# Kernel tuning notes

Measured on AMD Instinct MI355X. Metric: run time of the kernel, lower is better.

## Reference

```python
import jax, jax.numpy as jnp
import numpy as np

INPUT_SIZE, HIDDEN_SIZE, OUTPUT_SIZE = 256, 512, 256
BATCH, SEQ_LEN = 64, 1024


def _xavier(key, shape):
    fan_out, fan_in = shape
    limit = float(np.sqrt(6.0 / (fan_in + fan_out)))
    return jax.random.uniform(key, shape, jnp.float32, -limit, limit)


def setup_inputs() -> dict:
    key = jax.random.key(0)
    k_x, k_w1, k_w2 = jax.random.split(key, 3)
    x = jax.random.normal(k_x, (BATCH, SEQ_LEN, INPUT_SIZE), jnp.float32)
    W_ih = _xavier(k_w1, (HIDDEN_SIZE, INPUT_SIZE + HIDDEN_SIZE))  # torch Linear weight [out, in]
    b_ih = jnp.zeros((HIDDEN_SIZE,), jnp.float32)
    W_ho = _xavier(k_w2, (OUTPUT_SIZE, HIDDEN_SIZE))
    b_ho = jnp.zeros((OUTPUT_SIZE,), jnp.float32)
    return {"x": x, "W_ih": W_ih, "b_ih": b_ih, "W_ho": W_ho, "b_ho": b_ho}


def reference(x, W_ih, b_ih, W_ho, b_ho):
    batch, seq_len, input_size = x.shape
    hidden = W_ih.shape[0]
    # Split concat-linear into two matmuls: [x_t, h] @ W^T = x_t @ Wx^T + h @ Wh^T
    Wx = W_ih[:, :input_size]   # [H, I]
    Wh = W_ih[:, input_size:]   # [H, H]
    # Precompute input projections for all timesteps: [S, B, H]
    x_proj = jnp.einsum('bsi,hi->sbh', x, Wx) + b_ih

    def step(h, xp_t):
        h_new = jnp.tanh(xp_t + h @ Wh.T)
        return h_new, h_new

    h0 = jnp.zeros((batch, hidden), x.dtype)
    _, hs = jax.lax.scan(step, h0, x_proj)          # hs: [S, B, H]
    hidden_seq = jnp.transpose(hs, (1, 0, 2))       # [B, S, H]
    final_hidden = hidden_seq[:, -1, :]             # [B, H]
    scores = jnp.einsum('bsh,bh->bs', hidden_seq, final_hidden)
    attn = jax.nn.softmax(scores, axis=1)
    context = jnp.einsum('bs,bsh->bh', attn, hidden_seq)
    return context @ W_ho.T + b_ho
```

## Files before the change

### kernel.cpp

```cpp
#include <hip/hip_runtime.h>
#include <cstdint>
#include <cmath>

#define S_LEN 1024
#define BATCH 64
#define IN_SZ 256
#define HID 512
#define OUT_SZ 256
#define WIH_LD 768
#define BH (BATCH * HID)
#define XP_FLOATS (S_LEN * BH)

#define P_REG 176
#define P_LDS 24
#define P_STR_G 14


typedef _Float16 h2v __attribute__((ext_vector_type(2)));
typedef _Float16 f16x8 __attribute__((ext_vector_type(8)));
typedef float f32x4 __attribute__((ext_vector_type(4)));

__device__ __forceinline__ float dot2p(unsigned int a, unsigned int b, float c) {
#if __has_builtin(__builtin_amdgcn_fdot2)
    return __builtin_amdgcn_fdot2(__builtin_bit_cast(h2v, a),
                                  __builtin_bit_cast(h2v, b), c, false);
#else
    h2v av = __builtin_bit_cast(h2v, a);
    h2v bv = __builtin_bit_cast(h2v, b);
    return c + (float)av.x * (float)bv.x + (float)av.y * (float)bv.y;
#endif
}

__device__ __forceinline__ float fast_tanh(float x) {
    float e = __expf(2.0f * x);
#if __has_builtin(__builtin_amdgcn_rcpf)
    float r = __builtin_amdgcn_rcpf(e + 1.0f);
#else
    float r = 1.0f / (e + 1.0f);
#endif
    return __builtin_fmaf(-2.0f, r, 1.0f);
}

__global__ __launch_bounds__(256) void pack_w(const float* __restrict__ W_ih,
                                              unsigned int* __restrict__ wstr,
                                              unsigned int* __restrict__ wregbuf,
                                              unsigned int* __restrict__ wldsbuf) {
    int idx = blockIdx.x * 256 + threadIdx.x;
    int p = idx & 255;
    int j = idx >> 8;
    const float* src = W_ih + (size_t)j * WIH_LD + IN_SZ + 2 * p;
    unsigned short lo = __builtin_bit_cast(unsigned short, (_Float16)src[0]);
    unsigned short hi = __builtin_bit_cast(unsigned short, (_Float16)src[1]);
    unsigned int u = (unsigned int)lo | ((unsigned int)hi << 16);
    if (p < P_REG) {
        wregbuf[p * 512 + j] = u;
    } else if (p < P_REG + P_LDS) {
        wldsbuf[(p - P_REG) * 512 + j] = u;
    } else {
        int q = p - (P_REG + P_LDS);
        wstr[((q >> 2) * 512 + j) * 4 + (q & 3)] = u;
    }
}

__global__ __launch_bounds__(256) void pack_wf16(const float* __restrict__ W_ih,
                                                 uint4* __restrict__ wpk) {
    int idx = blockIdx.x * 256 + threadIdx.x;
    if (idx >= 16384) return;
    int nt   = idx >> 9;
    int ks   = (idx >> 6) & 7;
    int lane = idx & 63;
    int n  = nt * 16 + (lane & 15);
    int kb = ks * 32 + (lane >> 4) * 8;
    const float* src = W_ih + (size_t)n * WIH_LD + kb;
    union { uint4 u; _Float16 h[8]; } v;
#pragma unroll
    for (int i = 0; i < 8; ++i) v.h[i] = (_Float16)src[i];
    wpk[idx] = v.u;
}

#define AH_LD 264
__global__ __launch_bounds__(256) void xproj_mfma(const float* __restrict__ x,
                                                  const uint4* __restrict__ wpk,
                                                  const float* __restrict__ b_ih,
                                                  float* __restrict__ xp) {
    const int s    = blockIdx.x;
    const int half = blockIdx.y;
    const int tid  = threadIdx.x;
    __shared__ __align__(16) _Float16 Ah[32 * AH_LD];
    __shared__ float bsh[HID];
    bsh[tid] = b_ih[tid];
    bsh[tid + 256] = b_ih[tid + 256];
    {
        int r  = tid >> 3;
        int c0 = (tid & 7) * 32;
        const float4* s4 = (const float4*)(x + ((size_t)(half * 32 + r) * S_LEN + s) * IN_SZ + c0);
        _Float16* dst = &Ah[r * AH_LD + c0];
#pragma unroll
        for (int i = 0; i < 8; ++i) {
            float4 v = s4[i];
            dst[4 * i + 0] = (_Float16)v.x;
            dst[4 * i + 1] = (_Float16)v.y;
            dst[4 * i + 2] = (_Float16)v.z;
            dst[4 * i + 3] = (_Float16)v.w;
        }
    }
    __syncthreads();
    const int lane = tid & 63;
    const int w    = tid >> 6;
    const int mt   = w & 1;
    const int ntb  = (w >> 1) * 16;
    f16x8 areg[8];
#pragma unroll
    for (int ks = 0; ks < 8; ++ks)
        areg[ks] = *(const f16x8*)&Ah[(mt * 16 + (lane & 15)) * AH_LD + ks * 32 + (lane >> 4) * 8];
    const int brow  = half * 32 + mt * 16 + (lane >> 4) * 4;
    const int ncol0 = lane & 15;
    for (int nt2 = 0; nt2 < 16; ++nt2) {
        int nt = ntb + nt2;
        const uint4* bp = wpk + (size_t)nt * 8 * 64 + lane;
        f32x4 acc = {0.f, 0.f, 0.f, 0.f};
#pragma unroll
        for (int ks = 0; ks < 8; ++ks) {
            uint4 bu = bp[ks * 64];
            acc = __builtin_amdgcn_mfma_f32_16x16x32_f16(
                areg[ks], __builtin_bit_cast(f16x8, bu), acc, 0, 0, 0);
        }
        int n = nt * 16 + ncol0;
        float bias = bsh[n];
        float* outp = xp + (size_t)s * BH + (size_t)brow * HID + n;
#pragma unroll
        for (int r = 0; r < 4; ++r) outp[(size_t)r * HID] = acc[r] + bias;
    }
}

__global__ __launch_bounds__(512, 2) void rnn_f16(const unsigned int* __restrict__ wregbuf,
                                                  const unsigned int* __restrict__ wldsbuf,
                                                  const uint4* __restrict__ wstr,
                                                  float* __restrict__ xp) {
    const int b = blockIdx.x;
    const int j = threadIdx.x;

    __shared__ unsigned int wlds[P_LDS * 512];
    __shared__ unsigned short h2u[2][512];

    unsigned int wreg[P_REG];
#pragma unroll
    for (int p = 0; p < P_REG; ++p) wreg[p] = wregbuf[p * 512 + j];

    for (int g = j; g < P_LDS * 512; g += 512) wlds[g] = wldsbuf[g];
    h2u[0][j] = 0;
    __syncthreads();

    float* col = xp + (size_t)b * HID + j;
    for (int s = 0; s < S_LEN; ++s) {
        const unsigned int* hq = (const unsigned int*)h2u[s & 1];
        float xpv = col[(size_t)s * BH];

        uint4 sw[P_STR_G];
#pragma unroll
        for (int g = 0; g < P_STR_G; ++g) sw[g] = wstr[(size_t)g * 512 + j];

        float a0 = 0.f, a1 = 0.f, a2 = 0.f, a3 = 0.f;
#pragma unroll
        for (int p = 0; p < P_REG; p += 4) {
            a0 = dot2p(wreg[p + 0], hq[p + 0], a0);
            a1 = dot2p(wreg[p + 1], hq[p + 1], a1);
            a2 = dot2p(wreg[p + 2], hq[p + 2], a2);
            a3 = dot2p(wreg[p + 3], hq[p + 3], a3);
        }
#pragma unroll
        for (int p = 0; p < P_LDS; p += 4) {
            a0 = dot2p(wlds[(p + 0) * 512 + j], hq[P_REG + p + 0], a0);
            a1 = dot2p(wlds[(p + 1) * 512 + j], hq[P_REG + p + 1], a1);
            a2 = dot2p(wlds[(p + 2) * 512 + j], hq[P_REG + p + 2], a2);
            a3 = dot2p(wlds[(p + 3) * 512 + j], hq[P_REG + p + 3], a3);
        }
#pragma unroll
        for (int g = 0; g < P_STR_G; ++g) {
            int pb = P_REG + P_LDS + 4 * g;
            a0 = dot2p(sw[g].x, hq[pb + 0], a0);
            a1 = dot2p(sw[g].y, hq[pb + 1], a1);
            a2 = dot2p(sw[g].z, hq[pb + 2], a2);
            a3 = dot2p(sw[g].w, hq[pb + 3], a3);
        }

        float v = fast_tanh(((a0 + a1) + (a2 + a3)) + xpv);
        col[(size_t)s * BH] = v;
        h2u[(s + 1) & 1][j] = __builtin_bit_cast(unsigned short, (_Float16)v);
        asm volatile("s_waitcnt lgkmcnt(0)" ::: "memory");
        asm volatile("s_barrier" ::: "memory");
    }
}

__global__ __launch_bounds__(256) void attn_sc(const float* __restrict__ hbuf,
                                               float* __restrict__ sc_g) {
    const int b     = blockIdx.x;
    const int chunk = blockIdx.y;
    const int tid   = threadIdx.x;
    const int lane  = tid & 63;
    const int wv    = tid >> 6;
    __shared__ float fh[HID];
    fh[tid] = hbuf[(size_t)(S_LEN - 1) * BH + (size_t)b * HID + tid];
    fh[tid + 256] = hbuf[(size_t)(S_LEN - 1) * BH + (size_t)b * HID + tid + 256];
    __syncthreads();
    float4 f0 = *(const float4*)&fh[lane * 8];
    float4 f1 = *(const float4*)&fh[lane * 8 + 4];
    for (int i = 0; i < 32; ++i) {
        int s = chunk * 128 + wv * 32 + i;
        const float* hr = hbuf + (size_t)s * BH + (size_t)b * HID + lane * 8;
        float4 a0 = *(const float4*)hr;
        float4 a1 = *(const float4*)(hr + 4);
        float p = a0.x * f0.x + a0.y * f0.y + a0.z * f0.z + a0.w * f0.w +
                  a1.x * f1.x + a1.y * f1.y + a1.z * f1.z + a1.w * f1.w;
#pragma unroll
        for (int off = 32; off; off >>= 1) p += __shfl_down(p, off, 64);
        if (lane == 0) sc_g[(size_t)b * S_LEN + s] = p;
    }
}

__global__ __launch_bounds__(256) void attn_ctx(const float* __restrict__ hbuf,
                                                const float* __restrict__ sc_g,
                                                float* __restrict__ ctx_g) {
    const int b   = blockIdx.x;
    const int hc  = blockIdx.y * 128;
    const int tid = threadIdx.x;
    const int lane = tid & 63;
    const int wv   = tid >> 6;
    __shared__ float sc[S_LEN];
    __shared__ float red[4];
    __shared__ float part[256];
    for (int i = tid; i < S_LEN; i += 256) sc[i] = sc_g[(size_t)b * S_LEN + i];
    __syncthreads();
    float m = -1e30f;
    for (int i = tid; i < S_LEN; i += 256) m = fmaxf(m, sc[i]);
#pragma unroll
    for (int off = 32; off; off >>= 1) m = fmaxf(m, __shfl_down(m, off, 64));
    if (lane == 0) red[wv] = m;
    __syncthreads();
    m = fmaxf(fmaxf(red[0], red[1]), fmaxf(red[2], red[3]));
    float sum = 0.f;
    for (int i = tid; i < S_LEN; i += 256) {
        float e = __expf(sc[i] - m);
        sc[i] = e;
        sum += e;
    }
#pragma unroll
    for (int off = 32; off; off >>= 1) sum += __shfl_down(sum, off, 64);
    __syncthreads();
    if (lane == 0) red[wv] = sum;
    __syncthreads();
    float inv = 1.f / (red[0] + red[1] + red[2] + red[3]);
    const int h  = hc + (tid & 127);
    const int sh = tid >> 7;
    const float* hp = hbuf + (size_t)sh * 512 * BH + (size_t)b * HID + h;
    float c = 0.f;
#pragma unroll 4
    for (int s2 = 0; s2 < 512; ++s2)
        c += sc[sh * 512 + s2] * hp[(size_t)s2 * BH];
    part[tid] = c;
    __syncthreads();
    if (tid < 128) ctx_g[(size_t)b * HID + hc + tid] = (part[tid] + part[tid + 128]) * inv;
}

__global__ __launch_bounds__(256) void attn_fin(const float* __restrict__ ctx_g,
                                                const float* __restrict__ W_ho,
                                                const float* __restrict__ b_ho,
                                                float* __restrict__ out) {
    const int b   = blockIdx.x;
    const int tid = threadIdx.x;
    __shared__ float ctx[HID];
    ctx[tid] = ctx_g[(size_t)b * HID + tid];
    ctx[tid + 256] = ctx_g[(size_t)b * HID + tid + 256];
    __syncthreads();
    float o = b_ho[tid];
    const float* wr = W_ho + (size_t)tid * HID;
#pragma unroll 4
    for (int k = 0; k < HID; ++k) o += wr[k] * ctx[k];
    out[(size_t)b * OUT_SZ + tid] = o;
}

extern "C" void kernel_launch(void* const* d_in, const int* in_sizes, int n_in,
                              void* d_out, int out_size, void* d_ws, size_t ws_size,
                              hipStream_t stream) {
    const float* x    = (const float*)d_in[0];
    const float* W_ih = (const float*)d_in[1];
    const float* b_ih = (const float*)d_in[2];
    const float* W_ho = (const float*)d_in[3];
    const float* b_ho = (const float*)d_in[4];
    float* out = (float*)d_out;
    float* ws  = (float*)d_ws;

    float* xp = ws;
    unsigned int* wbase   = (unsigned int*)(ws + XP_FLOATS);
    unsigned int* wstr    = wbase;
    unsigned int* wregbuf = wbase + 28672;
    unsigned int* wldsbuf = wbase + 28672 + P_REG * 512;
    uint4*        wpk     = (uint4*)(wbase + 131072);
    float*        sc_g    = (float*)wbase;
    float*        ctx_g   = (float*)(wbase + 65536);

    pack_w<<<dim3(512), dim3(256), 0, stream>>>(W_ih, wstr, wregbuf, wldsbuf);
    pack_wf16<<<dim3(64), dim3(256), 0, stream>>>(W_ih, wpk);
    xproj_mfma<<<dim3(1024, 2), dim3(256), 0, stream>>>(x, wpk, b_ih, xp);
    rnn_f16<<<dim3(64), dim3(512), 0, stream>>>(wregbuf, wldsbuf, (const uint4*)wstr, xp);
    attn_sc<<<dim3(64, 8), dim3(256), 0, stream>>>(xp, sc_g);
    attn_ctx<<<dim3(64, 4), dim3(256), 0, stream>>>(xp, sc_g, ctx_g);
    attn_fin<<<dim3(64), dim3(256), 0, stream>>>(ctx_g, W_ho, b_ho, out);
}
```

Baseline: 1.758 ms.

## Move streamed recurrent weights into swizzled LDS and prefetch next-step input projection

The recurrent weight columns that were previously re-read from global memory on every timestep (14 uint4 per thread) now live in LDS. The LDS region grows from 24 to 76 packed words per column, in a per-thread contiguous, XOR-swizzled layout read with 128-bit LDS loads. The last 4 words are held in registers. The input projection for the next step is loaded one iteration ahead to hide its global latency inside the serial loop. The cost is about 152KB of LDS per block and a one-past-end read of the workspace on the final step.

```diff
diff --git a/kernel.cpp b/kernel.cpp
--- a/kernel.cpp
+++ b/kernel.cpp
@@ -12,8 +12,7 @@
 #define XP_FLOATS (S_LEN * BH)
 
 #define P_REG 176
-#define P_LDS 24
-#define P_STR_G 14
+#define P_LDS 76
 
 
 typedef _Float16 h2v __attribute__((ext_vector_type(2)));
@@ -55,10 +54,11 @@
     if (p < P_REG) {
         wregbuf[p * 512 + j] = u;
     } else if (p < P_REG + P_LDS) {
-        wldsbuf[(p - P_REG) * 512 + j] = u;
+        int w = (j * P_LDS + (p - P_REG)) ^ (((j >> 3) & 7) << 2);
+        wldsbuf[w] = u;
     } else {
         int q = p - (P_REG + P_LDS);
-        wstr[((q >> 2) * 512 + j) * 4 + (q & 3)] = u;
+        wstr[j * 4 + q] = u;
     }
 }
 
@@ -140,25 +140,26 @@
     const int b = blockIdx.x;
     const int j = threadIdx.x;
 
-    __shared__ unsigned int wlds[P_LDS * 512];
-    __shared__ unsigned short h2u[2][512];
+    __shared__ __align__(16) unsigned int wlds[P_LDS * 512];
+    __shared__ __align__(16) unsigned short h2u[2][512];
 
     unsigned int wreg[P_REG];
 #pragma unroll
     for (int p = 0; p < P_REG; ++p) wreg[p] = wregbuf[p * 512 + j];
-
-    for (int g = j; g < P_LDS * 512; g += 512) wlds[g] = wldsbuf[g];
+    const uint4 sw = wstr[j];
+
+    for (int w = j; w < P_LDS * 512; w += 512) wlds[w] = wldsbuf[w];
     h2u[0][j] = 0;
     __syncthreads();
 
+    const unsigned int swz   = ((j >> 3) & 7) << 2;
+    const unsigned int wbase = (unsigned int)j * P_LDS;
+
     float* col = xp + (size_t)b * HID + j;
+    float xpv = col[0];
     for (int s = 0; s < S_LEN; ++s) {
         const unsigned int* hq = (const unsigned int*)h2u[s & 1];
-        float xpv = col[(size_t)s * BH];
-
-        uint4 sw[P_STR_G];
-#pragma unroll
-        for (int g = 0; g < P_STR_G; ++g) sw[g] = wstr[(size_t)g * 512 + j];
+        float xpn = col[(size_t)(s + 1) * BH];
 
         float a0 = 0.f, a1 = 0.f, a2 = 0.f, a3 = 0.f;
 #pragma unroll
@@ -169,19 +170,21 @@
             a3 = dot2p(wreg[p + 3], hq[p + 3], a3);
         }
 #pragma unroll
-        for (int p = 0; p < P_LDS; p += 4) {
-            a0 = dot2p(wlds[(p + 0) * 512 + j], hq[P_REG + p + 0], a0);
-            a1 = dot2p(wlds[(p + 1) * 512 + j], hq[P_REG + p + 1], a1);
-            a2 = dot2p(wlds[(p + 2) * 512 + j], hq[P_REG + p + 2], a2);
-            a3 = dot2p(wlds[(p + 3) * 512 + j], hq[P_REG + p + 3], a3);
-        }
-#pragma unroll
-        for (int g = 0; g < P_STR_G; ++g) {
-            int pb = P_REG + P_LDS + 4 * g;
-            a0 = dot2p(sw[g].x, hq[pb + 0], a0);
-            a1 = dot2p(sw[g].y, hq[pb + 1], a1);
-            a2 = dot2p(sw[g].z, hq[pb + 2], a2);
-            a3 = dot2p(sw[g].w, hq[pb + 3], a3);
+        for (int kk = 0; kk < P_LDS / 4; ++kk) {
+            unsigned int w = (wbase + 4 * kk) ^ swz;
+            uint4 wv = *(const uint4*)&wlds[w];
+            int pb = P_REG + 4 * kk;
+            a0 = dot2p(wv.x, hq[pb + 0], a0);
+            a1 = dot2p(wv.y, hq[pb + 1], a1);
+            a2 = dot2p(wv.z, hq[pb + 2], a2);
+            a3 = dot2p(wv.w, hq[pb + 3], a3);
+        }
+        {
+            int pb = P_REG + P_LDS;
+            a0 = dot2p(sw.x, hq[pb + 0], a0);
+            a1 = dot2p(sw.y, hq[pb + 1], a1);
+            a2 = dot2p(sw.z, hq[pb + 2], a2);
+            a3 = dot2p(sw.w, hq[pb + 3], a3);
         }
 
         float v = fast_tanh(((a0 + a1) + (a2 + a3)) + xpv);
@@ -189,6 +192,7 @@
         h2u[(s + 1) & 1][j] = __builtin_bit_cast(unsigned short, (_Float16)v);
         asm volatile("s_waitcnt lgkmcnt(0)" ::: "memory");
         asm volatile("s_barrier" ::: "memory");
+        xpv = xpn;
     }
 }
 
@@ -293,8 +297,8 @@
     float* xp = ws;
     unsigned int* wbase   = (unsigned int*)(ws + XP_FLOATS);
     unsigned int* wstr    = wbase;
-    unsigned int* wregbuf = wbase + 28672;
-    unsigned int* wldsbuf = wbase + 28672 + P_REG * 512;
+    unsigned int* wregbuf = wbase + 2048;
+    unsigned int* wldsbuf = wbase + 2048 + P_REG * 512;
     uint4*        wpk     = (uint4*)(wbase + 131072);
     float*        sc_g    = (float*)wbase;
     float*        ctx_g   = (float*)(wbase + 65536);
```

Result: slower. 2.402 ms (+36.6%).

## Compute two hidden units per thread in RNN recurrence with 256-thread blocks

Applied to the files above, without the earlier changes.

The recurrent kernel now uses 256 threads per batch row, each computing two adjacent hidden units, so every 128-bit LDS read of the hidden state feeds twice as many dot products. Weight packing is reorganised into interleaved pairs, and the register/LDS/streamed split is rebalanced (136 in registers, 56 in LDS, 64 streamed from global) with vectorised LDS weight loads. Fewer waves per block should make the per-step barrier cheaper and reduce LDS traffic for h. In exchange each thread holds 272 weight registers plus a larger streamed buffer, which raises register pressure and spill risk, and per-thread serial work per step doubles.

```diff
diff --git a/kernel.cpp b/kernel.cpp
--- a/kernel.cpp
+++ b/kernel.cpp
@@ -11,9 +11,9 @@
 #define BH (BATCH * HID)
 #define XP_FLOATS (S_LEN * BH)
 
-#define P_REG 176
-#define P_LDS 24
-#define P_STR_G 14
+#define P_REG 136
+#define P_LDS 56
+#define P_STR 64
 
 
 typedef _Float16 h2v __attribute__((ext_vector_type(2)));
@@ -42,9 +42,9 @@
 }
 
 __global__ __launch_bounds__(256) void pack_w(const float* __restrict__ W_ih,
-                                              unsigned int* __restrict__ wstr,
-                                              unsigned int* __restrict__ wregbuf,
-                                              unsigned int* __restrict__ wldsbuf) {
+                                              unsigned int* __restrict__ wstr2,
+                                              unsigned int* __restrict__ wregbuf2,
+                                              unsigned int* __restrict__ wldsbuf2) {
     int idx = blockIdx.x * 256 + threadIdx.x;
     int p = idx & 255;
     int j = idx >> 8;
@@ -52,13 +52,20 @@
     unsigned short lo = __builtin_bit_cast(unsigned short, (_Float16)src[0]);
     unsigned short hi = __builtin_bit_cast(unsigned short, (_Float16)src[1]);
     unsigned int u = (unsigned int)lo | ((unsigned int)hi << 16);
+    int t = j >> 1;
+    int jj = j & 1;
     if (p < P_REG) {
-        wregbuf[p * 512 + j] = u;
+        wregbuf2[(p * 256 + t) * 2 + jj] = u;
     } else if (p < P_REG + P_LDS) {
-        wldsbuf[(p - P_REG) * 512 + j] = u;
+        int d  = p - P_REG;
+        int g2 = d >> 1;
+        int e  = d & 1;
+        wldsbuf2[(g2 * 256 + t) * 4 + jj * 2 + e] = u;
     } else {
         int q = p - (P_REG + P_LDS);
-        wstr[((q >> 2) * 512 + j) * 4 + (q & 3)] = u;
+        int g = q >> 2;
+        int c = q & 3;
+        wstr2[((g * 2 + jj) * 256 + t) * 4 + c] = u;
     }
 }
 
@@ -133,60 +140,93 @@
     }
 }
 
-__global__ __launch_bounds__(512, 2) void rnn_f16(const unsigned int* __restrict__ wregbuf,
-                                                  const unsigned int* __restrict__ wldsbuf,
-                                                  const uint4* __restrict__ wstr,
+__global__ __launch_bounds__(256, 1) void rnn_f16(const unsigned int* __restrict__ wregbuf2,
+                                                  const uint4* __restrict__ wldsbuf2,
+                                                  const uint4* __restrict__ wstr2,
                                                   float* __restrict__ xp) {
     const int b = blockIdx.x;
-    const int j = threadIdx.x;
-
-    __shared__ unsigned int wlds[P_LDS * 512];
-    __shared__ unsigned short h2u[2][512];
-
-    unsigned int wreg[P_REG];
-#pragma unroll
-    for (int p = 0; p < P_REG; ++p) wreg[p] = wregbuf[p * 512 + j];
-
-    for (int g = j; g < P_LDS * 512; g += 512) wlds[g] = wldsbuf[g];
-    h2u[0][j] = 0;
-    __syncthreads();
-
-    float* col = xp + (size_t)b * HID + j;
+    const int t = threadIdx.x;
+
+    __shared__ __align__(16) uint4 wlds[P_LDS / 2 * 256];
+    __shared__ __align__(16) unsigned int h2u[2][256];
+
+    unsigned int wregA[P_REG], wregB[P_REG];
+    {
+        const uint2* wr2 = (const uint2*)wregbuf2;
+#pragma unroll
+        for (int p = 0; p < P_REG; ++p) {
+            uint2 v = wr2[p * 256 + t];
+            wregA[p] = v.x;
+            wregB[p] = v.y;
+        }
+    }
+    for (int i = t; i < P_LDS / 2 * 256; i += 256) wlds[i] = wldsbuf2[i];
+    h2u[0][t] = 0;
+    __syncthreads();
+
+    float* col = xp + (size_t)b * HID + 2 * t;
     for (int s = 0; s < S_LEN; ++s) {
-        const unsigned int* hq = (const unsigned int*)h2u[s & 1];
-        float xpv = col[(size_t)s * BH];
-
-        uint4 sw[P_STR_G];
-#pragma unroll
-        for (int g = 0; g < P_STR_G; ++g) sw[g] = wstr[(size_t)g * 512 + j];
-
-        float a0 = 0.f, a1 = 0.f, a2 = 0.f, a3 = 0.f;
-#pragma unroll
-        for (int p = 0; p < P_REG; p += 4) {
-            a0 = dot2p(wreg[p + 0], hq[p + 0], a0);
-            a1 = dot2p(wreg[p + 1], hq[p + 1], a1);
-            a2 = dot2p(wreg[p + 2], hq[p + 2], a2);
-            a3 = dot2p(wreg[p + 3], hq[p + 3], a3);
-        }
-#pragma unroll
-        for (int p = 0; p < P_LDS; p += 4) {
-            a0 = dot2p(wlds[(p + 0) * 512 + j], hq[P_REG + p + 0], a0);
-            a1 = dot2p(wlds[(p + 1) * 512 + j], hq[P_REG + p + 1], a1);
-            a2 = dot2p(wlds[(p + 2) * 512 + j], hq[P_REG + p + 2], a2);
-            a3 = dot2p(wlds[(p + 3) * 512 + j], hq[P_REG + p + 3], a3);
-        }
-#pragma unroll
-        for (int g = 0; g < P_STR_G; ++g) {
-            int pb = P_REG + P_LDS + 4 * g;
-            a0 = dot2p(sw[g].x, hq[pb + 0], a0);
-            a1 = dot2p(sw[g].y, hq[pb + 1], a1);
-            a2 = dot2p(sw[g].z, hq[pb + 2], a2);
-            a3 = dot2p(sw[g].w, hq[pb + 3], a3);
-        }
-
-        float v = fast_tanh(((a0 + a1) + (a2 + a3)) + xpv);
-        col[(size_t)s * BH] = v;
-        h2u[(s + 1) & 1][j] = __builtin_bit_cast(unsigned short, (_Float16)v);
+        const uint4* hq4 = (const uint4*)&h2u[s & 1][0];
+        float2 xpv = *(const float2*)(col + (size_t)s * BH);
+
+        uint4 swA[16], swB[16];
+#pragma unroll
+        for (int g = 0; g < 16; ++g) {
+            swA[g] = wstr2[g * 512 + t];
+            swB[g] = wstr2[g * 512 + 256 + t];
+        }
+
+        float aA0 = 0.f, aA1 = 0.f, aA2 = 0.f, aA3 = 0.f;
+        float aB0 = 0.f, aB1 = 0.f, aB2 = 0.f, aB3 = 0.f;
+
+#pragma unroll
+        for (int g = 0; g < P_REG / 4; ++g) {
+            uint4 hh = hq4[g];
+            aA0 = dot2p(wregA[4 * g + 0], hh.x, aA0);
+            aA1 = dot2p(wregA[4 * g + 1], hh.y, aA1);
+            aA2 = dot2p(wregA[4 * g + 2], hh.z, aA2);
+            aA3 = dot2p(wregA[4 * g + 3], hh.w, aA3);
+            aB0 = dot2p(wregB[4 * g + 0], hh.x, aB0);
+            aB1 = dot2p(wregB[4 * g + 1], hh.y, aB1);
+            aB2 = dot2p(wregB[4 * g + 2], hh.z, aB2);
+            aB3 = dot2p(wregB[4 * g + 3], hh.w, aB3);
+        }
+#pragma unroll
+        for (int g = P_REG / 4; g < (P_REG + P_LDS) / 4; ++g) {
+            uint4 hh = hq4[g];
+            int g2 = 2 * (g - P_REG / 4);
+            uint4 wv0 = wlds[(g2 + 0) * 256 + t];
+            uint4 wv1 = wlds[(g2 + 1) * 256 + t];
+            aA0 = dot2p(wv0.x, hh.x, aA0);
+            aA1 = dot2p(wv0.y, hh.y, aA1);
+            aB0 = dot2p(wv0.z, hh.x, aB0);
+            aB1 = dot2p(wv0.w, hh.y, aB1);
+            aA2 = dot2p(wv1.x, hh.z, aA2);
+            aA3 = dot2p(wv1.y, hh.w, aA3);
+            aB2 = dot2p(wv1.z, hh.z, aB2);
+            aB3 = dot2p(wv1.w, hh.w, aB3);
+        }
+#pragma unroll
+        for (int k = 0; k < 16; ++k) {
+            uint4 hh = hq4[(P_REG + P_LDS) / 4 + k];
+            aA0 = dot2p(swA[k].x, hh.x, aA0);
+            aA1 = dot2p(swA[k].y, hh.y, aA1);
+            aA2 = dot2p(swA[k].z, hh.z, aA2);
+            aA3 = dot2p(swA[k].w, hh.w, aA3);
+            aB0 = dot2p(swB[k].x, hh.x, aB0);
+            aB1 = dot2p(swB[k].y, hh.y, aB1);
+            aB2 = dot2p(swB[k].z, hh.z, aB2);
+            aB3 = dot2p(swB[k].w, hh.w, aB3);
+        }
+
+        float vA = fast_tanh(((aA0 + aA1) + (aA2 + aA3)) + xpv.x);
+        float vB = fast_tanh(((aB0 + aB1) + (aB2 + aB3)) + xpv.y);
+        float2 out2 = {vA, vB};
+        *(float2*)(col + (size_t)s * BH) = out2;
+        unsigned int pk =
+            (unsigned int)__builtin_bit_cast(unsigned short, (_Float16)vA) |
+            ((unsigned int)__builtin_bit_cast(unsigned short, (_Float16)vB) << 16);
+        h2u[(s + 1) & 1][t] = pk;
         asm volatile("s_waitcnt lgkmcnt(0)" ::: "memory");
         asm volatile("s_barrier" ::: "memory");
     }
@@ -291,18 +331,19 @@
     float* ws  = (float*)d_ws;
 
     float* xp = ws;
-    unsigned int* wbase   = (unsigned int*)(ws + XP_FLOATS);
-    unsigned int* wstr    = wbase;
-    unsigned int* wregbuf = wbase + 28672;
-    unsigned int* wldsbuf = wbase + 28672 + P_REG * 512;
-    uint4*        wpk     = (uint4*)(wbase + 131072);
-    float*        sc_g    = (float*)wbase;
-    float*        ctx_g   = (float*)(wbase + 65536);
-
-    pack_w<<<dim3(512), dim3(256), 0, stream>>>(W_ih, wstr, wregbuf, wldsbuf);
+    unsigned int* wbase    = (unsigned int*)(ws + XP_FLOATS);
+    unsigned int* wstr2    = wbase;
+    unsigned int* wregbuf2 = wbase + 32768;
+    unsigned int* wldsbuf2 = wbase + 102400;
+    uint4*        wpk      = (uint4*)(wbase + 131072);
+    float*        sc_g     = (float*)wbase;
+    float*        ctx_g    = (float*)(wbase + 65536);
+
+    pack_w<<<dim3(512), dim3(256), 0, stream>>>(W_ih, wstr2, wregbuf2, wldsbuf2);
     pack_wf16<<<dim3(64), dim3(256), 0, stream>>>(W_ih, wpk);
     xproj_mfma<<<dim3(1024, 2), dim3(256), 0, stream>>>(x, wpk, b_ih, xp);
-    rnn_f16<<<dim3(64), dim3(512), 0, stream>>>(wregbuf, wldsbuf, (const uint4*)wstr, xp);
+    rnn_f16<<<dim3(64), dim3(256), 0, stream>>>(wregbuf2, (const uint4*)wldsbuf2,
+                                                (const uint4*)wstr2, xp);
     attn_sc<<<dim3(64, 8), dim3(256), 0, stream>>>(xp, sc_g);
     attn_ctx<<<dim3(64, 4), dim3(256), 0, stream>>>(xp, sc_g, ctx_g);
     attn_fin<<<dim3(64), dim3(256), 0, stream>>>(ctx_g, W_ho, b_ho, out);
```

Result: slower. 3.827 ms (+117.7%).

## Split each hidden unit's recurrent dot product across two threads

Applied to the files above, without the earlier changes.

The recurrent kernel now runs 1024 threads per batch row, with two threads per hidden unit. Each thread covers half of the 512-wide reduction and the halves are combined with a lane shuffle. Per-thread weights shrink to 64 registers, 32 uint4 in LDS and 32 streamed from global, and h is read from LDS as uint4 vectors. The goal is a shorter serial dependency chain per timestep and lower register pressure, paid for by a shuffle, idle lanes during the tanh/store step, and a 1024-thread barrier each step.

```diff
diff --git a/kernel.cpp b/kernel.cpp
--- a/kernel.cpp
+++ b/kernel.cpp
@@ -11,9 +11,6 @@
 #define BH (BATCH * HID)
 #define XP_FLOATS (S_LEN * BH)
 
-#define P_REG 176
-#define P_LDS 24
-#define P_STR_G 14
 
 
 typedef _Float16 h2v __attribute__((ext_vector_type(2)));
@@ -42,9 +39,9 @@
 }
 
 __global__ __launch_bounds__(256) void pack_w(const float* __restrict__ W_ih,
-                                              unsigned int* __restrict__ wstr,
-                                              unsigned int* __restrict__ wregbuf,
-                                              unsigned int* __restrict__ wldsbuf) {
+                                              unsigned int* __restrict__ wstr3,
+                                              unsigned int* __restrict__ wregbuf3,
+                                              unsigned int* __restrict__ wldsbuf3) {
     int idx = blockIdx.x * 256 + threadIdx.x;
     int p = idx & 255;
     int j = idx >> 8;
@@ -52,13 +49,16 @@
     unsigned short lo = __builtin_bit_cast(unsigned short, (_Float16)src[0]);
     unsigned short hi = __builtin_bit_cast(unsigned short, (_Float16)src[1]);
     unsigned int u = (unsigned int)lo | ((unsigned int)hi << 16);
-    if (p < P_REG) {
-        wregbuf[p * 512 + j] = u;
-    } else if (p < P_REG + P_LDS) {
-        wldsbuf[(p - P_REG) * 512 + j] = u;
+    int t = 2 * j + (p >> 7);
+    int q = p & 127;
+    int g = q >> 2;
+    int c = q & 3;
+    if (g < 16) {
+        wregbuf3[q * 1024 + t] = u;
+    } else if (g < 24) {
+        wldsbuf3[((g - 16) * 1024 + t) * 4 + c] = u;
     } else {
-        int q = p - (P_REG + P_LDS);
-        wstr[((q >> 2) * 512 + j) * 4 + (q & 3)] = u;
+        wstr3[t * 32 + (g - 24) * 4 + c] = u;
     }
 }
 
@@ -133,60 +133,76 @@
     }
 }
 
-__global__ __launch_bounds__(512, 2) void rnn_f16(const unsigned int* __restrict__ wregbuf,
-                                                  const unsigned int* __restrict__ wldsbuf,
-                                                  const uint4* __restrict__ wstr,
-                                                  float* __restrict__ xp) {
+__global__ __launch_bounds__(1024, 4) void rnn_f16(const unsigned int* __restrict__ wregbuf3,
+                                                   const uint4* __restrict__ wldsbuf3,
+                                                   const uint4* __restrict__ wstr3,
+                                                   float* __restrict__ xp) {
     const int b = blockIdx.x;
-    const int j = threadIdx.x;
-
-    __shared__ unsigned int wlds[P_LDS * 512];
-    __shared__ unsigned short h2u[2][512];
-
-    unsigned int wreg[P_REG];
-#pragma unroll
-    for (int p = 0; p < P_REG; ++p) wreg[p] = wregbuf[p * 512 + j];
-
-    for (int g = j; g < P_LDS * 512; g += 512) wlds[g] = wldsbuf[g];
-    h2u[0][j] = 0;
-    __syncthreads();
-
+    const int t = threadIdx.x;
+    const int j = t >> 1;
+    const int half = t & 1;
+
+    __shared__ __align__(16) uint4 wlds4[8 * 1024];
+    __shared__ __align__(16) unsigned short h16[2][512];
+
+    unsigned int wreg[64];
+#pragma unroll
+    for (int q = 0; q < 64; ++q) wreg[q] = wregbuf3[q * 1024 + t];
+
+    for (int i = t; i < 8 * 1024; i += 1024) wlds4[i] = wldsbuf3[i];
+    if (t < 512) h16[0][t] = 0;
+    __syncthreads();
+
+    const uint4* swp = wstr3 + (size_t)t * 8;
     float* col = xp + (size_t)b * HID + j;
+
     for (int s = 0; s < S_LEN; ++s) {
-        const unsigned int* hq = (const unsigned int*)h2u[s & 1];
-        float xpv = col[(size_t)s * BH];
-
-        uint4 sw[P_STR_G];
-#pragma unroll
-        for (int g = 0; g < P_STR_G; ++g) sw[g] = wstr[(size_t)g * 512 + j];
+        const uint4* hq4 = (const uint4*)&h16[s & 1][0];
+        const int hb = half * 32;
+
+        float xpv = 0.f;
+        if (half == 0) xpv = col[(size_t)s * BH];
+
+        uint4 sw[8];
+#pragma unroll
+        for (int g = 0; g < 8; ++g) sw[g] = swp[g];
 
         float a0 = 0.f, a1 = 0.f, a2 = 0.f, a3 = 0.f;
 #pragma unroll
-        for (int p = 0; p < P_REG; p += 4) {
-            a0 = dot2p(wreg[p + 0], hq[p + 0], a0);
-            a1 = dot2p(wreg[p + 1], hq[p + 1], a1);
-            a2 = dot2p(wreg[p + 2], hq[p + 2], a2);
-            a3 = dot2p(wreg[p + 3], hq[p + 3], a3);
-        }
-#pragma unroll
-        for (int p = 0; p < P_LDS; p += 4) {
-            a0 = dot2p(wlds[(p + 0) * 512 + j], hq[P_REG + p + 0], a0);
-            a1 = dot2p(wlds[(p + 1) * 512 + j], hq[P_REG + p + 1], a1);
-            a2 = dot2p(wlds[(p + 2) * 512 + j], hq[P_REG + p + 2], a2);
-            a3 = dot2p(wlds[(p + 3) * 512 + j], hq[P_REG + p + 3], a3);
-        }
-#pragma unroll
-        for (int g = 0; g < P_STR_G; ++g) {
-            int pb = P_REG + P_LDS + 4 * g;
-            a0 = dot2p(sw[g].x, hq[pb + 0], a0);
-            a1 = dot2p(sw[g].y, hq[pb + 1], a1);
-            a2 = dot2p(sw[g].z, hq[pb + 2], a2);
-            a3 = dot2p(sw[g].w, hq[pb + 3], a3);
-        }
-
-        float v = fast_tanh(((a0 + a1) + (a2 + a3)) + xpv);
-        col[(size_t)s * BH] = v;
-        h2u[(s + 1) & 1][j] = __builtin_bit_cast(unsigned short, (_Float16)v);
+        for (int g = 0; g < 16; ++g) {
+            uint4 hh = hq4[hb + g];
+            a0 = dot2p(wreg[4 * g + 0], hh.x, a0);
+            a1 = dot2p(wreg[4 * g + 1], hh.y, a1);
+            a2 = dot2p(wreg[4 * g + 2], hh.z, a2);
+            a3 = dot2p(wreg[4 * g + 3], hh.w, a3);
+        }
+#pragma unroll
+        for (int g = 0; g < 8; ++g) {
+            uint4 wv = wlds4[g * 1024 + t];
+            uint4 hh = hq4[hb + 16 + g];
+            a0 = dot2p(wv.x, hh.x, a0);
+            a1 = dot2p(wv.y, hh.y, a1);
+            a2 = dot2p(wv.z, hh.z, a2);
+            a3 = dot2p(wv.w, hh.w, a3);
+        }
+#pragma unroll
+        for (int g = 0; g < 8; ++g) {
+            uint4 hh = hq4[hb + 24 + g];
+            a0 = dot2p(sw[g].x, hh.x, a0);
+            a1 = dot2p(sw[g].y, hh.y, a1);
+            a2 = dot2p(sw[g].z, hh.z, a2);
+            a3 = dot2p(sw[g].w, hh.w, a3);
+        }
+
+        float partial = (a0 + a1) + (a2 + a3);
+        partial += __shfl_xor(partial, 1, 64);
+
+        if (half == 0) {
+            float v = fast_tanh(partial + xpv);
+            col[(size_t)s * BH] = v;
+            h16[(s + 1) & 1][j] =
+                __builtin_bit_cast(unsigned short, (_Float16)v);
+        }
         asm volatile("s_waitcnt lgkmcnt(0)" ::: "memory");
         asm volatile("s_barrier" ::: "memory");
     }
@@ -291,18 +307,19 @@
     float* ws  = (float*)d_ws;
 
     float* xp = ws;
-    unsigned int* wbase   = (unsigned int*)(ws + XP_FLOATS);
-    unsigned int* wstr    = wbase;
-    unsigned int* wregbuf = wbase + 28672;
-    unsigned int* wldsbuf = wbase + 28672 + P_REG * 512;
-    uint4*        wpk     = (uint4*)(wbase + 131072);
-    float*        sc_g    = (float*)wbase;
-    float*        ctx_g   = (float*)(wbase + 65536);
-
-    pack_w<<<dim3(512), dim3(256), 0, stream>>>(W_ih, wstr, wregbuf, wldsbuf);
+    unsigned int* wbase    = (unsigned int*)(ws + XP_FLOATS);
+    unsigned int* wstr3    = wbase;
+    unsigned int* wregbuf3 = wbase + 32768;
+    unsigned int* wldsbuf3 = wbase + 98304;
+    uint4*        wpk      = (uint4*)(wbase + 131072);
+    float*        sc_g     = (float*)wbase;
+    float*        ctx_g    = (float*)(wbase + 65536);
+
+    pack_w<<<dim3(512), dim3(256), 0, stream>>>(W_ih, wstr3, wregbuf3, wldsbuf3);
     pack_wf16<<<dim3(64), dim3(256), 0, stream>>>(W_ih, wpk);
     xproj_mfma<<<dim3(1024, 2), dim3(256), 0, stream>>>(x, wpk, b_ih, xp);
-    rnn_f16<<<dim3(64), dim3(512), 0, stream>>>(wregbuf, wldsbuf, (const uint4*)wstr, xp);
+    rnn_f16<<<dim3(64), dim3(1024), 0, stream>>>(wregbuf3, (const uint4*)wldsbuf3,
+                                                 (const uint4*)wstr3, xp);
     attn_sc<<<dim3(64, 8), dim3(256), 0, stream>>>(xp, sc_g);
     attn_ctx<<<dim3(64, 4), dim3(256), 0, stream>>>(xp, sc_g, ctx_g);
     attn_fin<<<dim3(64), dim3(256), 0, stream>>>(ctx_g, W_ho, b_ho, out);
```

Measured after the change: 2.654 ms. 1.51x slower.
